# Performance work log

Hardware: AMD Instinct MI355X
Metric: run time of the kernel (lower is better)

The kernel has to match this reference:

```python
import jax, jax.numpy as jnp
import numpy as np

N, C, E = 50000, 128, 10
INV3 = float(1.0 / np.sqrt(3.0))
NORM_C = float(1.0 / np.sqrt(C))


def setup_inputs() -> dict:
    key = jax.random.key(0)
    ks = jax.random.split(key, 14)
    node_feats = jax.random.normal(ks[0], (N, 4 * C), jnp.float32)
    elem = jax.random.randint(ks[1], (N,), 0, E)
    node_attrs = jax.nn.one_hot(elem, E, dtype=jnp.float32)
    sc = jax.random.normal(ks[2], (N, 4 * C), jnp.float32)
    tp2_w = jax.random.normal(ks[3], (4, C), jnp.float32)
    tp3_w = jax.random.normal(ks[4], (8, C), jnp.float32)
    coef0_w0 = jax.random.normal(ks[5], (E, C, C), jnp.float32)
    coef0_w1 = jax.random.normal(ks[6], (E, C, C), jnp.float32)
    coef1_w0 = jax.random.normal(ks[7], (E, 2 * C, C), jnp.float32)
    coef1_w1 = jax.random.normal(ks[8], (E, 2 * C, C), jnp.float32)
    coef2_w0 = jax.random.normal(ks[9], (E, 4 * C, C), jnp.float32)
    coef2_w1 = jax.random.normal(ks[10], (E, 4 * C, C), jnp.float32)
    lin_w0 = jax.random.normal(ks[11], (C, C), jnp.float32)
    lin_w1 = jax.random.normal(ks[12], (C, C), jnp.float32)
    return dict(node_feats=node_feats, node_attrs=node_attrs, sc=sc,
                tp2_w=tp2_w, tp3_w=tp3_w,
                coef0_w0=coef0_w0, coef0_w1=coef0_w1,
                coef1_w0=coef1_w0, coef1_w1=coef1_w1,
                coef2_w0=coef2_w0, coef2_w1=coef2_w1,
                lin_w0=lin_w0, lin_w1=lin_w1)


def acc_elem_linear(x0, x1, attrs, W0, W1):
    # per-element linear combine: one-hot attrs select element-specific weights
    norm = 1.0 / np.sqrt(x0.shape[1])
    o0 = jnp.zeros((attrs.shape[0], W0.shape[2]), x0.dtype)
    o1 = jnp.zeros((attrs.shape[0], W1.shape[2], 3), x1.dtype)
    for e in range(W0.shape[0]):  # small fixed element count
        a = attrs[:, e]
        o0 = o0 + a[:, None] * (x0 @ W0[e])
        o1 = o1 + a[:, None, None] * jnp.einsum('ncm,cd->ndm', x1, W1[e])
    return o0 * norm, o1 * norm


def reference(node_feats, node_attrs, sc, tp2_w, tp3_w,
              coef0_w0, coef0_w1, coef1_w0, coef1_w1,
              coef2_w0, coef2_w1, lin_w0, lin_w1):
    n = node_feats.shape[0]
    s = node_feats[:, :C]                      # [N,C]    0e
    v = node_feats[:, C:].reshape(n, C, 3)     # [N,C,3]  1o

    # nu=2: channelwise (uuu) CG tensor product, paths filtered to {0e,1o}
    m0a = tp2_w[0] * s * s                                # 0e x 0e -> 0e
    m1a = tp2_w[1][:, None] * s[:, :, None] * v * INV3    # 0e x 1o -> 1o
    m1b = tp2_w[2][:, None] * v * s[:, :, None] * INV3    # 1o x 0e -> 1o
    m0b = tp2_w[3] * jnp.sum(v * v, axis=-1) * INV3       # 1o x 1o -> 0e

    # nu=3: mid (A0=m0a 0e, A1=m1a 1o, A2=m1b 1o, A3=m0b 0e) x node_feats
    q0 = jnp.concatenate([
        tp3_w[0] * m0a * s,
        tp3_w[3] * jnp.sum(m1a * v, -1) * INV3,
        tp3_w[5] * jnp.sum(m1b * v, -1) * INV3,
        tp3_w[6] * m0b * s], axis=1)                      # [N,4C]
    q1 = jnp.concatenate([
        tp3_w[1][:, None] * m0a[:, :, None] * v * INV3,
        tp3_w[2][:, None] * m1a * s[:, :, None] * INV3,
        tp3_w[4][:, None] * m1b * s[:, :, None] * INV3,
        tp3_w[7][:, None] * m0b[:, :, None] * v * INV3], axis=1)  # [N,4C,3]

    f0, f1 = acc_elem_linear(s, v, node_attrs, coef0_w0, coef0_w1)
    g0, g1 = acc_elem_linear(jnp.concatenate([m0a, m0b], 1),
                             jnp.concatenate([m1a, m1b], 1),
                             node_attrs, coef1_w0, coef1_w1)
    h0, h1 = acc_elem_linear(q0, q1, node_attrs, coef2_w0, coef2_w1)
    o0 = f0 + g0 + h0
    o1 = f1 + g1 + h1

    o0 = (o0 @ lin_w0) * NORM_C
    o1 = jnp.einsum('ncm,cd->ndm', o1, lin_w1) * NORM_C
    out = jnp.concatenate([o0, o1.reshape(n, -1)], axis=1) + sc
    return out
```

## Files before the change

kernel.cpp:

```cpp
#include <hip/hip_runtime.h>

typedef unsigned short u16;
typedef __attribute__((ext_vector_type(8))) short short8;
typedef __attribute__((ext_vector_type(4))) float f32x4;

#define N_NODES 50000
#define C_ 128
#define E_ 10
#define NT_ 16
#define NBLK_MAIN 3200
#define K0_ 640
#define K1_ 512

#define WF0_BYTES (E_ * 8 * 20 * 512 * 2)
#define WF1_BYTES (E_ * 8 * 16 * 512 * 2)
#define CNT_OFF   (WF0_BYTES + WF1_BYTES)
#define LIST_OFF  (CNT_OFF + 64)

__device__ __forceinline__ u16 f2bf(float f){ union{unsigned u; float f;} v; v.f = f; unsigned u = v.u; u += 0x7FFFu + ((u>>16)&1u); return (u16)(u>>16); }
__device__ __forceinline__ unsigned cvtpk(float a, float b){
    unsigned r;
    asm("v_cvt_pk_bf16_f32 %0, %1, %2" : "=v"(r) : "v"(a), "v"(b));
    return r;
}

__global__ __launch_bounds__(256) void prep_weights_kernel(
    const float* __restrict__ tp2, const float* __restrict__ tp3,
    const float* __restrict__ c00, const float* __restrict__ c10, const float* __restrict__ c20,
    const float* __restrict__ c01, const float* __restrict__ c11, const float* __restrict__ c21,
    const float* __restrict__ lin0, const float* __restrict__ lin1,
    u16* __restrict__ WF0, u16* __restrict__ WF1)
{
    const int b = blockIdx.x;
    const int e = b / 9, kb = b % 9;
    const int which = (kb >= 5) ? 1 : 0;
    const int seg = which ? kb - 5 : kb;
    const float* __restrict__ lin = which ? lin1 : lin0;

    __shared__ u16 R[128 * 136];
    __shared__ u16 LT[128 * 132];

    const int tid = threadIdx.x;
    const float NC = 0.08838834764831845f;

    for (int t = tid; t < 128 * 32; t += 256) {
        const int jj = t >> 5, c4 = (t & 31) << 2;
        const float4 v = *(const float4*)(lin + jj * 128 + c4);
        LT[(c4 + 0) * 132 + jj] = f2bf(v.x * NC);
        LT[(c4 + 1) * 132 + jj] = f2bf(v.y * NC);
        LT[(c4 + 2) * 132 + jj] = f2bf(v.z * NC);
        LT[(c4 + 3) * 132 + jj] = f2bf(v.w * NC);
    }

    {
        const int c = tid >> 1, jh = (tid & 1) * 64;
        const float i128 = 0.08838834764831845f;
        const float i256 = 0.0625f;
        const float i512 = 0.04419417382415922f;
        const float I3   = 0.5773502691896258f;
        const float I9   = I3 * I3;
        const float t2_0 = tp2[0*C_+c], t2_1 = tp2[1*C_+c], t2_2 = tp2[2*C_+c], t2_3 = tp2[3*C_+c];
        const float t3_0 = tp3[0*C_+c], t3_1 = tp3[1*C_+c], t3_2 = tp3[2*C_+c];
        const float t3_3 = tp3[3*C_+c], t3_4 = tp3[4*C_+c], t3_5 = tp3[5*C_+c];
        const float t3_6 = tp3[6*C_+c], t3_7 = tp3[7*C_+c];

        const float* P0; const float* P1 = nullptr; const float* P2 = nullptr;
        float a0 = 0.f, a1 = 0.f, a2 = 0.f;
        if (!which) {
            const float* C0 = c00 + (size_t)e * C_   * C_;
            const float* C1 = c10 + (size_t)e * 2*C_ * C_;
            const float* C2 = c20 + (size_t)e * 4*C_ * C_;
            switch (seg) {
            case 0: P0 = C0 + c*C_;          a0 = i128; break;
            case 1: P0 = C1 + c*C_;          a0 = t2_0 * i256; break;
            case 2: P0 = C1 + (C_+c)*C_;     a0 = t2_3 * I3 * i256; break;
            case 3: P0 = C2 + c*C_;          a0 = t3_0 * t2_0 * i512; break;
            default:
                P0 = C2 + (C_+c)*C_;         a0 = t3_3 * t2_1 * I9 * i512;
                P1 = C2 + (2*C_+c)*C_;       a1 = t3_5 * t2_2 * I9 * i512;
                P2 = C2 + (3*C_+c)*C_;       a2 = t3_6 * t2_3 * I3 * i512; break;
            }
        } else {
            const float* C0 = c01 + (size_t)e * C_   * C_;
            const float* C1 = c11 + (size_t)e * 2*C_ * C_;
            const float* C2 = c21 + (size_t)e * 4*C_ * C_;
            switch (seg) {
            case 0: P0 = C0 + c*C_;          a0 = i128; break;
            case 1: P0 = C1 + c*C_;          a0 = t2_1 * I3 * i256;
                    P1 = C1 + (C_+c)*C_;     a1 = t2_2 * I3 * i256; break;
            case 2: P0 = C2 + c*C_;          a0 = t3_1 * t2_0 * I3 * i512;
                    P1 = C2 + (C_+c)*C_;     a1 = t3_2 * t2_1 * I9 * i512;
                    P2 = C2 + (2*C_+c)*C_;   a2 = t3_4 * t2_2 * I9 * i512; break;
            default: P0 = C2 + (3*C_+c)*C_;  a0 = t3_7 * t2_3 * I9 * i512; break;
            }
        }
        for (int j4 = 0; j4 < 64; j4 += 4) {
            const int jj = jh + j4;
            const float4 v = *(const float4*)(P0 + jj);
            float r0 = a0*v.x, r1 = a0*v.y, r2 = a0*v.z, r3 = a0*v.w;
            if (P1) {
                const float4 u = *(const float4*)(P1 + jj);
                r0 += a1*u.x; r1 += a1*u.y; r2 += a1*u.z; r3 += a1*u.w;
            }
            if (P2) {
                const float4 u = *(const float4*)(P2 + jj);
                r0 += a2*u.x; r1 += a2*u.y; r2 += a2*u.z; r3 += a2*u.w;
            }
            ushort4 st; st.x = f2bf(r0); st.y = f2bf(r1); st.z = f2bf(r2); st.w = f2bf(r3);
            *(ushort4*)&R[c * 136 + jj] = st;
        }
    }
    __syncthreads();

    const int wv = tid >> 6, l = tid & 63;
    const int lcol = l & 15, gD = l >> 4;
    f32x4 acc[2][8];
#pragma unroll
    for (int s = 0; s < 2; ++s)
#pragma unroll
        for (int t = 0; t < 8; ++t) acc[s][t] = (f32x4){0.f, 0.f, 0.f, 0.f};

#pragma unroll
    for (int ks2 = 0; ks2 < 4; ++ks2) {
        const int jj0 = ks2 * 32 + gD * 4;
        short8 bf[8];
#pragma unroll
        for (int t = 0; t < 8; ++t) {
            const int colB = t * 16 + lcol;
            union { unsigned long long q[2]; short8 v; } u;
            u.q[0] = *(const unsigned long long*)&LT[colB * 132 + jj0];
            u.q[1] = *(const unsigned long long*)&LT[colB * 132 + jj0 + 16];
            bf[t] = u.v;
        }
#pragma unroll
        for (int s = 0; s < 2; ++s) {
            const int krow = (wv + s * 4) * 16 + lcol;
            union { unsigned long long q[2]; short8 v; } ua;
            ua.q[0] = *(const unsigned long long*)&R[krow * 136 + jj0];
            ua.q[1] = *(const unsigned long long*)&R[krow * 136 + jj0 + 16];
#pragma unroll
            for (int t = 0; t < 8; ++t)
                acc[s][t] = __builtin_amdgcn_mfma_f32_16x16x32_bf16(ua.v, bf[t], acc[s][t], 0, 0, 0);
        }
    }

#pragma unroll
    for (int s = 0; s < 2; ++s) {
#pragma unroll
        for (int r = 0; r < 4; ++r) {
            const int k = (wv + s * 4) * 16 + 4 * gD + r;
            const int ks = k >> 5, r2 = k & 31;
            const int eh = r2 >> 4, g2 = (r2 >> 2) & 3, el = r2 & 3;
            const int elem = eh * 4 + el;
            const int lanef = lcol + 16 * g2;
            const int slot = seg * 4 + ks;
#pragma unroll
            for (int t = 0; t < 8; ++t) {
                const u16 wvl = f2bf(acc[s][t][r]);
                if (!which) WF0[(((size_t)(e*8 + t))*20 + slot)*512 + lanef*8 + elem] = wvl;
                else        WF1[(((size_t)(e*8 + t))*16 + slot)*512 + lanef*8 + elem] = wvl;
            }
        }
    }
}

__global__ void bucket_kernel(const float* __restrict__ attrs,
                              int* __restrict__ cnt, int* __restrict__ lists)
{
    __shared__ int lcnt[E_];
    __shared__ int lbase[E_];
    const int n = blockIdx.x * 256 + threadIdx.x;
    if (threadIdx.x < E_) lcnt[threadIdx.x] = 0;
    __syncthreads();
    int e = 0, my = 0;
    if (n < N_NODES) {
        const float* a = attrs + (size_t)n * E_;
#pragma unroll
        for (int i = 0; i < E_; ++i) if (a[i] > 0.5f) e = i;
        my = atomicAdd(&lcnt[e], 1);
    }
    __syncthreads();
    if (threadIdx.x < E_) lbase[threadIdx.x] = atomicAdd(&cnt[threadIdx.x], lcnt[threadIdx.x]);
    __syncthreads();
    if (n < N_NODES) lists[e*N_NODES + lbase[e] + my] = n;
}

__global__ __launch_bounds__(256, 3) void main_kernel(
    const float* __restrict__ feats, const float* __restrict__ sc,
    const int* __restrict__ cnt, const int* __restrict__ lists,
    const u16* __restrict__ WF0, const u16* __restrict__ WF1,
    float* __restrict__ out)
{
    __shared__ __align__(16) u16 A2[2][24 * 512];

    const int tid = threadIdx.x;
    const int bx = blockIdx.x;

    int e = -1, tile = 0, accT = 0;
#pragma unroll
    for (int i = 0; i < E_; ++i) {
        const int ci = cnt[i];
        const int t = (ci + NT_ - 1) >> 4;
        if (e < 0 && bx < accT + t) { e = i; tile = bx - accT; }
        accT += t;
    }
    if (e < 0) return;
    const int nvalid = min(NT_, cnt[e] - tile * NT_);

    const int node = tid >> 4;
    const int cg   = tid & 15;
    const int n = (node < nvalid) ? lists[e*N_NODES + tile*NT_ + node] : -1;

    float4 s0 = make_float4(0.f,0.f,0.f,0.f), s1 = s0;
    float4 v4[6];
#pragma unroll
    for (int k = 0; k < 6; ++k) v4[k] = s0;
    if (n >= 0) {
        const float* f = feats + (size_t)n * 512;
        s0 = *(const float4*)(f + cg*8);
        s1 = *(const float4*)(f + cg*8 + 4);
#pragma unroll
        for (int k = 0; k < 6; ++k) v4[k] = *(const float4*)(f + 128 + cg*24 + 4*k);
    }
    float S[8]  = {s0.x,s0.y,s0.z,s0.w, s1.x,s1.y,s1.z,s1.w};
    float V[24] = {v4[0].x,v4[0].y,v4[0].z,v4[0].w, v4[1].x,v4[1].y,v4[1].z,v4[1].w,
                   v4[2].x,v4[2].y,v4[2].z,v4[2].w, v4[3].x,v4[3].y,v4[3].z,v4[3].w,
                   v4[4].x,v4[4].y,v4[4].z,v4[4].w, v4[5].x,v4[5].y,v4[5].z,v4[5].w};
    float S2[8], VV[8];
#pragma unroll
    for (int i = 0; i < 8; ++i) {
        S2[i] = S[i]*S[i];
        VV[i] = V[3*i]*V[3*i] + V[3*i+1]*V[3*i+1] + V[3*i+2]*V[3*i+2];
    }

    const int ksl   = cg >> 2;
    const int eh    = (cg >> 1) & 1;
    const int gb    = (cg & 1) * 2;
    const int lp0   = (node + 16*gb)        ^ (ksl << 1);
    const int lp1   = (node + 16*(gb + 1))  ^ (ksl << 1);
    const int off0  = lp0*8 + 4*eh;
    const int off1  = lp1*8 + 4*eh;

#define WSLOT(BUF, SLOT, V0,V1,V2,V3,V4,V5,V6,V7) do { \
        uint2 w0_, w1_; \
        w0_.x = cvtpk((V0),(V1)); w0_.y = cvtpk((V2),(V3)); \
        w1_.x = cvtpk((V4),(V5)); w1_.y = cvtpk((V6),(V7)); \
        *(uint2*)&A2[BUF][(SLOT)*512 + off0] = w0_; \
        *(uint2*)&A2[BUF][(SLOT)*512 + off1] = w1_; \
    } while (0)

    WSLOT(0, 0*4 + ksl, S[0],S[1],S[2],S[3],S[4],S[5],S[6],S[7]);
    WSLOT(0, 1*4 + ksl, S2[0],S2[1],S2[2],S2[3],S2[4],S2[5],S2[6],S2[7]);
    WSLOT(0, 2*4 + ksl, VV[0],VV[1],VV[2],VV[3],VV[4],VV[5],VV[6],VV[7]);
    WSLOT(0, 3*4 + ksl, S2[0]*S[0],S2[1]*S[1],S2[2]*S[2],S2[3]*S[3],
                        S2[4]*S[4],S2[5]*S[5],S2[6]*S[6],S2[7]*S[7]);
    WSLOT(0, 4*4 + ksl, S[0]*VV[0],S[1]*VV[1],S[2]*VV[2],S[3]*VV[3],
                        S[4]*VV[4],S[5]*VV[5],S[6]*VV[6],S[7]*VV[7]);
    __syncthreads();

    const int w4 = tid >> 6, l = tid & 63;
    const int lcol = l & 15, g = l >> 4;
    const int col0 = (2*w4)*16 + lcol;
    const int col1 = col0 + 16;
    const u16* WB0a = WF0 + ((size_t)(e*8 + 2*w4))     * (20*512) + l*8;
    const u16* WB0b = WB0a + 20*512;
    const u16* WB1a = WF1 + ((size_t)(e*8 + 2*w4))     * (16*512) + l*8;
    const u16* WB1b = WB1a + 16*512;

    f32x4 accS0 = {0.f,0.f,0.f,0.f}, accS1 = accS0;
    f32x4 accV[3][2];
#pragma unroll
    for (int m = 0; m < 3; ++m) { accV[m][0] = accS0; accV[m][1] = accS0; }

#pragma unroll
    for (int m = 0; m < 3; ++m) {
        WSLOT(1, m*4 + ksl,     V[0*3+m],V[1*3+m],V[2*3+m],V[3*3+m],
                                V[4*3+m],V[5*3+m],V[6*3+m],V[7*3+m]);
        WSLOT(1, (3+m)*4 + ksl, S[0]*V[0*3+m],S[1]*V[1*3+m],S[2]*V[2*3+m],S[3]*V[3*3+m],
                                S[4]*V[4*3+m],S[5]*V[5*3+m],S[6]*V[6*3+m],S[7]*V[7*3+m]);
    }
#pragma unroll
    for (int ks2 = 0; ks2 < 4; ++ks2) {
        const int lp8 = (l ^ (ks2 << 1)) * 8;
#pragma unroll
        for (int p = 0; p < 5; ++p) {
            const short8 a  = *(const short8*)&A2[0][(p*4 + ks2)*512 + lp8];
            const short8 b0 = *(const short8*)(WB0a + (p*4 + ks2)*512);
            const short8 b1 = *(const short8*)(WB0b + (p*4 + ks2)*512);
            accS0 = __builtin_amdgcn_mfma_f32_16x16x32_bf16(a, b0, accS0, 0, 0, 0);
            accS1 = __builtin_amdgcn_mfma_f32_16x16x32_bf16(a, b1, accS1, 0, 0, 0);
        }
    }
    __syncthreads();

#pragma unroll
    for (int m = 0; m < 3; ++m) {
        WSLOT(0, m*4 + ksl,     S2[0]*V[0*3+m],S2[1]*V[1*3+m],S2[2]*V[2*3+m],S2[3]*V[3*3+m],
                                S2[4]*V[4*3+m],S2[5]*V[5*3+m],S2[6]*V[6*3+m],S2[7]*V[7*3+m]);
        WSLOT(0, (3+m)*4 + ksl, VV[0]*V[0*3+m],VV[1]*V[1*3+m],VV[2]*V[2*3+m],VV[3]*V[3*3+m],
                                VV[4]*V[4*3+m],VV[5]*V[5*3+m],VV[6]*V[6*3+m],VV[7]*V[7*3+m]);
    }
    float4 scR[8];
#pragma unroll
    for (int j = 0; j < 8; ++j) scR[j] = make_float4(0.f,0.f,0.f,0.f);
    if (n >= 0) {
        const float* sp = sc + (size_t)n * 512 + cg * 4;
#pragma unroll
        for (int j = 0; j < 8; ++j) scR[j] = *(const float4*)(sp + 64*j);
    }
#pragma unroll
    for (int ks2 = 0; ks2 < 4; ++ks2) {
        const int lp8 = (l ^ (ks2 << 1)) * 8;
#pragma unroll
        for (int q = 0; q < 2; ++q) {
            const short8 b0 = *(const short8*)(WB1a + (q*4 + ks2)*512);
            const short8 b1 = *(const short8*)(WB1b + (q*4 + ks2)*512);
#pragma unroll
            for (int m = 0; m < 3; ++m) {
                const short8 a = *(const short8*)&A2[1][((q*3 + m)*4 + ks2)*512 + lp8];
                accV[m][0] = __builtin_amdgcn_mfma_f32_16x16x32_bf16(a, b0, accV[m][0], 0, 0, 0);
                accV[m][1] = __builtin_amdgcn_mfma_f32_16x16x32_bf16(a, b1, accV[m][1], 0, 0, 0);
            }
        }
    }
    __syncthreads();

#pragma unroll
    for (int ks2 = 0; ks2 < 4; ++ks2) {
        const int lp8 = (l ^ (ks2 << 1)) * 8;
#pragma unroll
        for (int q = 0; q < 2; ++q) {
            const short8 b0 = *(const short8*)(WB1a + ((2+q)*4 + ks2)*512);
            const short8 b1 = *(const short8*)(WB1b + ((2+q)*4 + ks2)*512);
#pragma unroll
            for (int m = 0; m < 3; ++m) {
                const short8 a = *(const short8*)&A2[0][((q*3 + m)*4 + ks2)*512 + lp8];
                accV[m][0] = __builtin_amdgcn_mfma_f32_16x16x32_bf16(a, b0, accV[m][0], 0, 0, 0);
                accV[m][1] = __builtin_amdgcn_mfma_f32_16x16x32_bf16(a, b1, accV[m][1], 0, 0, 0);
            }
        }
    }
    __syncthreads();

    float* OutB = (float*)&A2[0][0];
#pragma unroll
    for (int r = 0; r < 4; ++r) {
        const int nd = 4*g + r;
        OutB[nd*516 + col0] = accS0[r];
        OutB[nd*516 + col1] = accS1[r];
#pragma unroll
        for (int m = 0; m < 3; ++m) {
            OutB[nd*516 + 128 + 3*col0 + m] = accV[m][0][r];
            OutB[nd*516 + 128 + 3*col1 + m] = accV[m][1][r];
        }
    }
    __syncthreads();

    if (n >= 0) {
        const size_t gb2 = (size_t)n * 512 + cg * 4;
#pragma unroll
        for (int j = 0; j < 8; ++j) {
            const float4 vres = *(const float4*)&OutB[node*516 + cg*4 + 64*j];
            float4 o;
            o.x = vres.x + scR[j].x; o.y = vres.y + scR[j].y;
            o.z = vres.z + scR[j].z; o.w = vres.w + scR[j].w;
            *(float4*)(out + gb2 + 64*j) = o;
        }
    }
#undef WSLOT
}

extern "C" void kernel_launch(void* const* d_in, const int* in_sizes, int n_in,
                              void* d_out, int out_size, void* d_ws, size_t ws_size,
                              hipStream_t stream) {
    const float* feats = (const float*)d_in[0];
    const float* attrs = (const float*)d_in[1];
    const float* sc    = (const float*)d_in[2];
    const float* tp2   = (const float*)d_in[3];
    const float* tp3   = (const float*)d_in[4];
    const float* c00   = (const float*)d_in[5];
    const float* c01   = (const float*)d_in[6];
    const float* c10   = (const float*)d_in[7];
    const float* c11   = (const float*)d_in[8];
    const float* c20   = (const float*)d_in[9];
    const float* c21   = (const float*)d_in[10];
    const float* lin0  = (const float*)d_in[11];
    const float* lin1  = (const float*)d_in[12];
    float* out = (float*)d_out;

    char* ws = (char*)d_ws;
    u16* WF0   = (u16*)(ws);
    u16* WF1   = (u16*)(ws + WF0_BYTES);
    int* cnt   = (int*)(ws + CNT_OFF);
    int* lists = (int*)(ws + LIST_OFF);

    hipMemsetAsync(cnt, 0, 64, stream);
    hipLaunchKernelGGL(prep_weights_kernel, dim3(E_*9), dim3(256), 0, stream,
                       tp2, tp3, c00, c10, c20, c01, c11, c21, lin0, lin1, WF0, WF1);
    hipLaunchKernelGGL(bucket_kernel, dim3((N_NODES + 255)/256), dim3(256), 0, stream,
                       attrs, cnt, lists);
    hipLaunchKernelGGL(main_kernel, dim3(NBLK_MAIN), dim3(256), 0, stream,
                       feats, sc, cnt, lists, WF0, WF1, out);
}
```

Baseline: 116.6 us.

## Make node bucketing deterministic via count/scan/scatter and swizzle block order

Replaces the atomic single-pass bucketing with three kernels: per-block element counts, a serial per-element prefix scan, and a scatter that ranks nodes with wave ballots. Node lists therefore come out in ascending node order within each element, which should make the feature and sc reads in the main kernel more contiguous. The hipMemset is dropped. The main kernel's block index is also remapped so that consecutive hardware blocks are spread across tiles, presumably to balance element groups across XCDs. This adds two extra kernel launches and a single-thread serial scan in exchange.

```diff
diff --git a/kernel.cpp b/kernel.cpp
--- a/kernel.cpp
+++ b/kernel.cpp
@@ -9,13 +9,16 @@
 #define E_ 10
 #define NT_ 16
 #define NBLK_MAIN 3200
+#define NBLK_S 196
 #define K0_ 640
 #define K1_ 512
 
 #define WF0_BYTES (E_ * 8 * 20 * 512 * 2)
 #define WF1_BYTES (E_ * 8 * 16 * 512 * 2)
-#define CNT_OFF   (WF0_BYTES + WF1_BYTES)
-#define LIST_OFF  (CNT_OFF + 64)
+#define CNT_OFF    (WF0_BYTES + WF1_BYTES)
+#define BLKCNT_OFF (CNT_OFF + 64)
+#define BASE_OFF   (BLKCNT_OFF + 8192)
+#define LIST_OFF   (BASE_OFF + 8192)
 
 __device__ __forceinline__ u16 f2bf(float f){ union{unsigned u; float f;} v; v.f = f; unsigned u = v.u; u += 0x7FFFu + ((u>>16)&1u); return (u16)(u>>16); }
 __device__ __forceinline__ unsigned cvtpk(float a, float b){
@@ -164,25 +167,62 @@
     }
 }
 
-__global__ void bucket_kernel(const float* __restrict__ attrs,
-                              int* __restrict__ cnt, int* __restrict__ lists)
-{
+__global__ void count_kernel(const float* __restrict__ attrs, int* __restrict__ blkcnt) {
     __shared__ int lcnt[E_];
-    __shared__ int lbase[E_];
-    const int n = blockIdx.x * 256 + threadIdx.x;
-    if (threadIdx.x < E_) lcnt[threadIdx.x] = 0;
-    __syncthreads();
-    int e = 0, my = 0;
+    const int blk = blockIdx.x, tid = threadIdx.x;
+    if (tid < E_) lcnt[tid] = 0;
+    __syncthreads();
+    const int n = blk * 256 + tid;
     if (n < N_NODES) {
         const float* a = attrs + (size_t)n * E_;
+        int e = 0;
 #pragma unroll
         for (int i = 0; i < E_; ++i) if (a[i] > 0.5f) e = i;
-        my = atomicAdd(&lcnt[e], 1);
-    }
-    __syncthreads();
-    if (threadIdx.x < E_) lbase[threadIdx.x] = atomicAdd(&cnt[threadIdx.x], lcnt[threadIdx.x]);
-    __syncthreads();
-    if (n < N_NODES) lists[e*N_NODES + lbase[e] + my] = n;
+        atomicAdd(&lcnt[e], 1);
+    }
+    __syncthreads();
+    if (tid < E_) blkcnt[tid * 200 + blk] = lcnt[tid];
+}
+
+__global__ void scan_kernel(const int* __restrict__ blkcnt, int* __restrict__ base,
+                            int* __restrict__ cnt) {
+    const int e = threadIdx.x;
+    if (e < E_) {
+        int acc = 0;
+        for (int b = 0; b < NBLK_S; ++b) { base[e * 200 + b] = acc; acc += blkcnt[e * 200 + b]; }
+        cnt[e] = acc;
+    }
+}
+
+__global__ void scatter_kernel(const float* __restrict__ attrs, const int* __restrict__ base,
+                               int* __restrict__ lists) {
+    __shared__ int wcnt[4][E_];
+    __shared__ int wbase[4][E_];
+    const int blk = blockIdx.x, tid = threadIdx.x;
+    const int wv = tid >> 6, lane = tid & 63;
+    const int n = blk * 256 + tid;
+    int e = -1;
+    if (n < N_NODES) {
+        e = 0;
+        const float* a = attrs + (size_t)n * E_;
+#pragma unroll
+        for (int i = 0; i < E_; ++i) if (a[i] > 0.5f) e = i;
+    }
+    int rank = 0;
+#pragma unroll
+    for (int v = 0; v < E_; ++v) {
+        const unsigned long long m = __ballot(e == v);
+        if (e == v) rank = __popcll(m & ((1ull << lane) - 1ull));
+        if (lane == 0) wcnt[wv][v] = __popcll(m);
+    }
+    __syncthreads();
+    if (tid < E_) {
+        int acc = 0;
+#pragma unroll
+        for (int w2 = 0; w2 < 4; ++w2) { wbase[w2][tid] = acc; acc += wcnt[w2][tid]; }
+    }
+    __syncthreads();
+    if (n < N_NODES) lists[e * N_NODES + base[e * 200 + blk] + wbase[wv][e] + rank] = n;
 }
 
 __global__ __launch_bounds__(256, 3) void main_kernel(
@@ -194,7 +234,8 @@
     __shared__ __align__(16) u16 A2[2][24 * 512];
 
     const int tid = threadIdx.x;
-    const int bx = blockIdx.x;
+    const int bxr = blockIdx.x;
+    const int bx = (bxr & 7) * (NBLK_MAIN / 8) + (bxr >> 3);
 
     int e = -1, tile = 0, accT = 0;
 #pragma unroll
@@ -389,16 +430,18 @@
     float* out = (float*)d_out;
 
     char* ws = (char*)d_ws;
-    u16* WF0   = (u16*)(ws);
-    u16* WF1   = (u16*)(ws + WF0_BYTES);
-    int* cnt   = (int*)(ws + CNT_OFF);
-    int* lists = (int*)(ws + LIST_OFF);
-
-    hipMemsetAsync(cnt, 0, 64, stream);
+    u16* WF0    = (u16*)(ws);
+    u16* WF1    = (u16*)(ws + WF0_BYTES);
+    int* cnt    = (int*)(ws + CNT_OFF);
+    int* blkcnt = (int*)(ws + BLKCNT_OFF);
+    int* base   = (int*)(ws + BASE_OFF);
+    int* lists  = (int*)(ws + LIST_OFF);
+
     hipLaunchKernelGGL(prep_weights_kernel, dim3(E_*9), dim3(256), 0, stream,
                        tp2, tp3, c00, c10, c20, c01, c11, c21, lin0, lin1, WF0, WF1);
-    hipLaunchKernelGGL(bucket_kernel, dim3((N_NODES + 255)/256), dim3(256), 0, stream,
-                       attrs, cnt, lists);
+    hipLaunchKernelGGL(count_kernel, dim3(NBLK_S), dim3(256), 0, stream, attrs, blkcnt);
+    hipLaunchKernelGGL(scan_kernel, dim3(1), dim3(64), 0, stream, blkcnt, base, cnt);
+    hipLaunchKernelGGL(scatter_kernel, dim3(NBLK_S), dim3(256), 0, stream, attrs, base, lists);
     hipLaunchKernelGGL(main_kernel, dim3(NBLK_MAIN), dim3(256), 0, stream,
                        feats, sc, cnt, lists, WF0, WF1, out);
 }
```

After: 119.5 us. +2.4%, slower.
